# Optimization experiments

Measured on AMD Instinct MI355X. Metric: run time of the kernel, lower is better.

The kernel has to match this reference:

```python
import jax, jax.numpy as jnp
import numpy as np

HEADS = 2
K_HOP = 2
RATIO = 0.8
NEG_SLOPE = 0.01


def seg_softmax(logits, seg, num_seg):
    # torch_geometric.utils.softmax: numerically stable segment softmax
    m = jax.ops.segment_max(logits, seg, num_segments=num_seg)
    e = jnp.exp(logits - m[seg])
    d = jax.ops.segment_sum(e, seg, num_segments=num_seg)
    return e / d[seg]


def _attention(key_value, query, seg, num_seg, Wk, W1, W2, W3):
    # Attention.forward with enable_BN=False; weights stored [in,out] so x@W == torch Linear
    a = key_value @ Wk
    h = jnp.concatenate([a, query, a - query, a * query], axis=-1)  # [N,4H]
    h = jax.nn.leaky_relu(h @ W1, NEG_SLOPE)
    h = jax.nn.leaky_relu(h @ W2, NEG_SLOPE)
    h = jax.nn.leaky_relu(h @ W3, NEG_SLOPE)  # [N,1]
    return seg_softmax(h[:, 0], seg, num_seg)[:, None]  # att_weights [N,1]


def setup_inputs():
    key = jax.random.key(0)
    ks = jax.random.split(key, 10)
    B, n, H, epg = 64, 64, 128, 2048
    N = B * n
    x = jax.random.normal(ks[0], (N, H), jnp.float32)
    src = jax.random.randint(ks[1], (B, epg), 0, n)
    dst = jax.random.randint(ks[2], (B, epg), 0, n)
    off = (jnp.arange(B) * n)[:, None]
    edge_index = jnp.stack([(src + off).reshape(-1), (dst + off).reshape(-1)], 0)
    edge_weight = jax.random.uniform(ks[3], (B * epg,), jnp.float32)
    target_x = jax.random.normal(ks[4], (B, H), jnp.float32)
    batch_ixs = jnp.repeat(jnp.arange(B), n)
    s = lambda i, sh: jax.random.normal(ks[i], sh, jnp.float32) / np.sqrt(sh[-2])
    # index 0=cluster_att, 1=query_att, 2=cluster_att2, 3=query_att2
    att_Wk = s(5, (4, H, H))
    att_W1 = s(6, (4, 4 * H, 2 * H))
    att_W2 = s(7, (4, 2 * H, H))
    att_W3 = s(8, (4, H, 1))
    lin_W = s(9, (HEADS, H, H))
    return dict(x=x, edge_index=edge_index, edge_weight=edge_weight, target_x=target_x,
                batch_ixs=batch_ixs, att_Wk=att_Wk, att_W1=att_W1, att_W2=att_W2,
                att_W3=att_W3, lin_W=lin_W)


def reference(x, edge_index, edge_weight, target_x, batch_ixs, att_Wk, att_W1, att_W2, att_W3, lin_W):
    N, H = x.shape
    B = target_x.shape[0]
    n = N // B
    # ---- gcn_norm with self loops (fill 1.0) ----
    loop = jnp.arange(N)
    row = jnp.concatenate([edge_index[0], loop])
    col = jnp.concatenate([edge_index[1], loop])
    w = jnp.concatenate([edge_weight, jnp.ones((N,), edge_weight.dtype)])
    deg = jax.ops.segment_sum(w, col, num_segments=N)
    dinv = jnp.where(deg > 0, jax.lax.rsqrt(jnp.maximum(deg, 1e-12)), 0.0)
    ew = dinv[row] * w * dinv[col]  # [L]
    # ---- k-hop propagation ----
    def hop(v):
        return jax.ops.segment_sum(v[row] * ew[:, None], col, num_segments=N)
    x_q = x
    for _ in range(K_HOP):
        x_q = hop(x_q)
    qt = target_x[batch_ixs]  # repeat_interleave by per-graph counts (sorted batch)
    # ---- multi-head edge attention (reuse_att_w=True, dropout=0 -> E identical per head) ----
    f1 = _attention(x, x_q, batch_ixs, B, att_Wk[0], att_W1[0], att_W2[0], att_W3[0])
    f2 = _attention(x, qt, batch_ixs, B, att_Wk[1], att_W1[1], att_W2[1], att_W3[1])
    E = jax.nn.leaky_relu(f1[col] + f2[row], NEG_SLOPE)  # [L,1]
    E = seg_softmax(E[:, 0], col, N)[:, None]
    x_c = jnp.zeros_like(x)
    E_g = jnp.zeros((row.shape[0], 1), x.dtype)
    agg = jax.ops.segment_sum(x[row] * E, col, num_segments=N)
    for h in range(HEADS):
        x_c = x_c + jax.nn.leaky_relu(x + agg @ lin_W[h], NEG_SLOPE)
        E_g = E_g + E
    x_c = x_c / HEADS
    E_g = E_g / HEADS
    # ---- second k-hop + cluster scoring ----
    x_q2 = x_c
    for _ in range(K_HOP):
        x_q2 = hop(x_q2)
    g1 = _attention(x_c, x_q2, batch_ixs, B, att_Wk[2], att_W1[2], att_W2[2], att_W3[2])
    g2 = _attention(x_c, qt, batch_ixs, B, att_Wk[3], att_W1[3], att_W2[3], att_W3[3])
    # stack over heads then mean == g1+g2 (same attention modules reused per head)
    cluster_score = seg_softmax((g1 + g2)[:, 0], batch_ixs, B)  # [N]
    # ---- per-graph topk (ratio) ----
    kk = int(np.ceil(RATIO * n))
    _, idx = jax.lax.top_k(cluster_score.reshape(B, n), kk)  # descending, matches PyG topk
    perm = (idx + (jnp.arange(B) * n)[:, None]).reshape(-1)  # [Nk]
    x_out = x[perm] * cluster_score[perm][:, None]
    batch_out = batch_ixs[perm]
    # ---- S^T A S (dense equivalent of SparseTensor triple product) ----
    A_d = jnp.zeros((N, N), x.dtype).at[row, col].add(ew)
    S_d = jnp.zeros((N, N), x.dtype).at[row, col].add(E_g[:, 0])
    S_p = S_d[:, perm]  # S[:, perm] -> [N, Nk]
    A2 = S_p.T @ (A_d @ S_p)  # [Nk, Nk]
    Nk = perm.shape[0]
    A2 = A2.at[jnp.arange(Nk), jnp.arange(Nk)].set(1.0)  # fill_diag(1.0)
    return x_out, A2, batch_out, perm
```

## Files before the change

kernel.cpp:

```cpp
#include <hip/hip_runtime.h>

#define KK 52
#define NKOUT 3328
#define NEG 0.01f

typedef __attribute__((ext_vector_type(8))) __bf16 bf16x8;
typedef __attribute__((ext_vector_type(16))) float floatx16;

__device__ __forceinline__ float lrelu(float v){ return v > 0.f ? v : NEG*v; }

#define SW(r, ko) ((r)*40 + ((ko) ^ ((((r)>>3)&3) << 3)))

__device__ __forceinline__ void split_store8(const float* vv, __bf16* P0, __bf16* P1, __bf16* P2, int addr){
  bf16x8 p1, p2, p3;
  #pragma unroll
  for (int j = 0; j < 8; j++){
    __bf16 b1 = (__bf16)vv[j];
    float r1 = vv[j] - (float)b1;
    __bf16 b2 = (__bf16)r1;
    float r2 = r1 - (float)b2;
    p1[j] = b1; p2[j] = b2; p3[j] = (__bf16)r2;
  }
  *(bf16x8*)(P0 + addr) = p1;
  *(bf16x8*)(P1 + addr) = p2;
  *(bf16x8*)(P2 + addr) = p3;
}

__device__ __forceinline__ void mfma6(const __bf16* A0, const __bf16* A1, const __bf16* A2,
                                      const __bf16* B0, const __bf16* B1, const __bf16* B2,
                                      int aoff, int boff, floatx16* acc){
  bf16x8 a1 = *(const bf16x8*)(A0 + aoff);
  bf16x8 a2 = *(const bf16x8*)(A1 + aoff);
  bf16x8 a3 = *(const bf16x8*)(A2 + aoff);
  bf16x8 b1 = *(const bf16x8*)(B0 + boff);
  bf16x8 b2 = *(const bf16x8*)(B1 + boff);
  bf16x8 b3 = *(const bf16x8*)(B2 + boff);
  floatx16 c = *acc;
  c = __builtin_amdgcn_mfma_f32_32x32x16_bf16(a1,b1,c,0,0,0);
  c = __builtin_amdgcn_mfma_f32_32x32x16_bf16(a1,b2,c,0,0,0);
  c = __builtin_amdgcn_mfma_f32_32x32x16_bf16(a2,b1,c,0,0,0);
  c = __builtin_amdgcn_mfma_f32_32x32x16_bf16(a1,b3,c,0,0,0);
  c = __builtin_amdgcn_mfma_f32_32x32x16_bf16(a3,b1,c,0,0,0);
  c = __builtin_amdgcn_mfma_f32_32x32x16_bf16(a2,b2,c,0,0,0);
  *acc = c;
}

__device__ __forceinline__ void g_gemm(const float* A0, int ldA,
                                       const float* __restrict__ W0, int ldW, int K,
                                       __bf16* pb, floatx16* oA, floatx16* oB){
  __bf16 *As0 = pb, *As1 = pb+2560, *As2 = pb+5120;
  __bf16 *Bs0 = pb+7680, *Bs1 = pb+12800, *Bs2 = pb+17920;
  int tid = threadIdx.x;
  int sar = tid >> 2, sako = (tid & 3)*8;
  int bn = tid & 127, bk = (tid >> 7)*16;
  int wv_ = tid >> 6, L = tid & 63, m = L & 31, half = L >> 5;
  int rA = 32*(wv_ & 1) + m, rB0 = (wv_ >> 1)*32 + m, rB1 = rB0 + 64;
  const float* arow = A0 + (size_t)sar*ldA;
  floatx16 accA, accB;
  #pragma unroll
  for (int i = 0; i < 16; i++){ accA[i] = 0.f; accB[i] = 0.f; }
  float ra[8], wv[16];
  {
    float4 v0 = *(const float4*)(arow + sako);
    float4 v1 = *(const float4*)(arow + sako + 4);
    ra[0]=v0.x; ra[1]=v0.y; ra[2]=v0.z; ra[3]=v0.w; ra[4]=v1.x; ra[5]=v1.y; ra[6]=v1.z; ra[7]=v1.w;
    #pragma unroll
    for (int j = 0; j < 16; j++) wv[j] = W0[(size_t)(bk + j)*ldW + bn];
  }
  for (int k0 = 0; k0 < K; k0 += 32){
    split_store8(ra, As0, As1, As2, SW(sar, sako));
    split_store8(wv,     Bs0, Bs1, Bs2, SW(bn, bk));
    split_store8(wv + 8, Bs0, Bs1, Bs2, SW(bn, bk + 8));
    __syncthreads();
    int k1 = k0 + 32;
    float ra2[8], wv2[16];
    if (k1 < K){
      float4 v0 = *(const float4*)(arow + k1 + sako);
      float4 v1 = *(const float4*)(arow + k1 + sako + 4);
      ra2[0]=v0.x; ra2[1]=v0.y; ra2[2]=v0.z; ra2[3]=v0.w; ra2[4]=v1.x; ra2[5]=v1.y; ra2[6]=v1.z; ra2[7]=v1.w;
      #pragma unroll
      for (int j = 0; j < 16; j++) wv2[j] = W0[(size_t)(k1 + bk + j)*ldW + bn];
    }
    #pragma unroll
    for (int kg = 0; kg < 2; kg++){
      int ko = kg*16 + half*8;
      mfma6(As0,As1,As2, Bs0,Bs1,Bs2, SW(rA,ko), SW(rB0,ko), &accA);
      mfma6(As0,As1,As2, Bs0,Bs1,Bs2, SW(rA,ko), SW(rB1,ko), &accB);
    }
    __syncthreads();
    if (k1 < K){
      #pragma unroll
      for (int j = 0; j < 8; j++) ra[j] = ra2[j];
      #pragma unroll
      for (int j = 0; j < 16; j++) wv[j] = wv2[j];
    }
  }
  *oA = accA; *oB = accB;
}

__device__ __forceinline__ void g_gemm64(const float* __restrict__ A0, int ldA,
                                         const float* __restrict__ W0, int ldW, int K,
                                         __bf16* pb, floatx16* oC){
  __bf16 *As0 = pb, *As1 = pb+2560, *As2 = pb+5120;
  __bf16 *Bs0 = pb+7680, *Bs1 = pb+10240, *Bs2 = pb+12800;
  int tid = threadIdx.x;
  int sar = tid >> 2, sako = (tid & 3)*8;
  int bn = tid & 63, bk = (tid >> 6)*8;
  int wv_ = tid >> 6, L = tid & 63, m = L & 31, half = L >> 5;
  int rA = 32*(wv_ & 1) + m, rB = 32*(wv_ >> 1) + m;
  const float* arow = A0 + (size_t)sar*ldA;
  floatx16 acc;
  #pragma unroll
  for (int i = 0; i < 16; i++) acc[i] = 0.f;
  float ra[8], wv[8];
  {
    float4 v0 = *(const float4*)(arow + sako);
    float4 v1 = *(const float4*)(arow + sako + 4);
    ra[0]=v0.x; ra[1]=v0.y; ra[2]=v0.z; ra[3]=v0.w; ra[4]=v1.x; ra[5]=v1.y; ra[6]=v1.z; ra[7]=v1.w;
    #pragma unroll
    for (int j = 0; j < 8; j++) wv[j] = W0[(size_t)(bk + j)*ldW + bn];
  }
  for (int k0 = 0; k0 < K; k0 += 32){
    split_store8(ra, As0, As1, As2, SW(sar, sako));
    split_store8(wv, Bs0, Bs1, Bs2, SW(bn, bk));
    __syncthreads();
    int k1 = k0 + 32;
    float ra2[8], wv2[8];
    if (k1 < K){
      float4 v0 = *(const float4*)(arow + k1 + sako);
      float4 v1 = *(const float4*)(arow + k1 + sako + 4);
      ra2[0]=v0.x; ra2[1]=v0.y; ra2[2]=v0.z; ra2[3]=v0.w; ra2[4]=v1.x; ra2[5]=v1.y; ra2[6]=v1.z; ra2[7]=v1.w;
      #pragma unroll
      for (int j = 0; j < 8; j++) wv2[j] = W0[(size_t)(k1 + bk + j)*ldW + bn];
    }
    #pragma unroll
    for (int kg = 0; kg < 2; kg++){
      int ko = kg*16 + half*8;
      mfma6(As0,As1,As2, Bs0,Bs1,Bs2, SW(rA,ko), SW(rB,ko), &acc);
    }
    __syncthreads();
    if (k1 < K){
      #pragma unroll
      for (int j = 0; j < 8; j++){ ra[j] = ra2[j]; wv[j] = wv2[j]; }
    }
  }
  *oC = acc;
}

__device__ __forceinline__ void g_gemm_h64(const float* __restrict__ arow, const float* __restrict__ qrow,
                                           const float* __restrict__ W1fz, int colbase,
                                           __bf16* pb, floatx16* oC){
  __bf16 *As0 = pb, *As1 = pb+2560, *As2 = pb+5120;
  __bf16 *Bs0 = pb+7680, *Bs1 = pb+10240, *Bs2 = pb+12800;
  int tid = threadIdx.x;
  int sar = tid >> 2, sako = (tid & 3)*8;
  int bn = tid & 63, bk = (tid >> 6)*8;
  int col = colbase + bn;
  int wv_ = tid >> 6, L = tid & 63, m = L & 31, half = L >> 5;
  int rA = 32*(wv_ & 1) + m, rB = 32*(wv_ >> 1) + m;
  auto loadA = [&](int k0, float* r){
    int seg = k0 >> 7, kl = (k0 & 127) + sako;
    if (seg == 0){
      float4 a0 = *(const float4*)(arow + kl), a1 = *(const float4*)(arow + kl + 4);
      r[0]=a0.x; r[1]=a0.y; r[2]=a0.z; r[3]=a0.w; r[4]=a1.x; r[5]=a1.y; r[6]=a1.z; r[7]=a1.w;
    } else if (seg == 1){
      float4 q0 = *(const float4*)(qrow + kl), q1 = *(const float4*)(qrow + kl + 4);
      r[0]=q0.x; r[1]=q0.y; r[2]=q0.z; r[3]=q0.w; r[4]=q1.x; r[5]=q1.y; r[6]=q1.z; r[7]=q1.w;
    } else {
      float4 a0 = *(const float4*)(arow + kl), a1 = *(const float4*)(arow + kl + 4);
      float4 q0 = *(const float4*)(qrow + kl), q1 = *(const float4*)(qrow + kl + 4);
      r[0]=a0.x*q0.x; r[1]=a0.y*q0.y; r[2]=a0.z*q0.z; r[3]=a0.w*q0.w;
      r[4]=a1.x*q1.x; r[5]=a1.y*q1.y; r[6]=a1.z*q1.z; r[7]=a1.w*q1.w;
    }
  };
  auto loadB = [&](int k0, float* r){
    #pragma unroll
    for (int j = 0; j < 8; j++) r[j] = W1fz[(size_t)(k0 + bk + j)*256 + col];
  };
  floatx16 acc;
  #pragma unroll
  for (int i = 0; i < 16; i++) acc[i] = 0.f;
  float ra[8], wv[8];
  loadA(0, ra); loadB(0, wv);
  for (int k0 = 0; k0 < 384; k0 += 32){
    split_store8(ra, As0, As1, As2, SW(sar, sako));
    split_store8(wv, Bs0, Bs1, Bs2, SW(bn, bk));
    __syncthreads();
    int k1 = k0 + 32;
    float ra2[8], wv2[8];
    if (k1 < 384){ loadA(k1, ra2); loadB(k1, wv2); }
    #pragma unroll
    for (int kg = 0; kg < 2; kg++){
      int ko = kg*16 + half*8;
      mfma6(As0,As1,As2, Bs0,Bs1,Bs2, SW(rA,ko), SW(rB,ko), &acc);
    }
    __syncthreads();
    if (k1 < 384){
      #pragma unroll
      for (int j = 0; j < 8; j++){ ra[j] = ra2[j]; wv[j] = wv2[j]; }
    }
  }
  *oC = acc;
}

__device__ __forceinline__ void c_write(floatx16 accA, floatx16 accB, float* C0, int ldC, int act){
  int tid = threadIdx.x, wv_ = tid >> 6, L = tid & 63, m = L & 31, half = L >> 5;
  int rB0 = (wv_ >> 1)*32 + m, rB1 = rB0 + 64;
  int row0 = 32*(wv_ & 1) + 4*half;
  #pragma unroll
  for (int reg = 0; reg < 16; reg++){
    int row = row0 + (reg & 3) + 8*(reg >> 2);
    float va = accA[reg], vb = accB[reg];
    if (act){ va = lrelu(va); vb = lrelu(vb); }
    C0[(size_t)row*ldC + rB0] = va;
    C0[(size_t)row*ldC + rB1] = vb;
  }
}

__device__ __forceinline__ void c_write64(floatx16 acc, float* C0, int ldC, int act){
  int tid = threadIdx.x, wv_ = tid >> 6, L = tid & 63, m = L & 31, half = L >> 5;
  int col = 32*(wv_ >> 1) + m;
  int row0 = 32*(wv_ & 1) + 4*half;
  #pragma unroll
  for (int reg = 0; reg < 16; reg++){
    int row = row0 + (reg & 3) + 8*(reg >> 2);
    float v = acc[reg];
    if (act) v = lrelu(v);
    C0[(size_t)row*ldC + col] = v;
  }
}

__device__ __forceinline__ void hop2_run(const float* A, const float* VfullL, int ldV,
                                         const float* srcG, float* dstG, int dstOff,
                                         float* Vt, float* Tt, int fbeg, int fend){
  int tid = threadIdx.x;
  int tc = (tid & 31)*2, tf = (tid >> 5)*4;
  for (int f0 = fbeg; f0 < fend; f0 += 32){
    if (!VfullL){
      for (int o = tid; o < 2048; o += 256){
        int r = o >> 5, f = o & 31;
        Vt[o] = srcG[r*128 + f0 + f];
      }
      __syncthreads();
    }
    float a00,a01,a02,a03,a10,a11,a12,a13;
    a00=a01=a02=a03=a10=a11=a12=a13=0.f;
    for (int r = 0; r < 64; r++){
      float x0 = A[r*64 + tc], x1 = A[r*64 + tc + 1];
      float4 v4 = VfullL ? *(const float4*)&VfullL[r*ldV + f0 + tf]
                         : *(const float4*)&Vt[r*32 + tf];
      a00 += x0*v4.x; a01 += x0*v4.y; a02 += x0*v4.z; a03 += x0*v4.w;
      a10 += x1*v4.x; a11 += x1*v4.y; a12 += x1*v4.z; a13 += x1*v4.w;
    }
    *(float4*)&Tt[tc*32 + tf]     = make_float4(a00,a01,a02,a03);
    *(float4*)&Tt[(tc+1)*32 + tf] = make_float4(a10,a11,a12,a13);
    __syncthreads();
    a00=a01=a02=a03=a10=a11=a12=a13=0.f;
    for (int r = 0; r < 64; r++){
      float x0 = A[r*64 + tc], x1 = A[r*64 + tc + 1];
      float4 v4 = *(const float4*)&Tt[r*32 + tf];
      a00 += x0*v4.x; a01 += x0*v4.y; a02 += x0*v4.z; a03 += x0*v4.w;
      a10 += x1*v4.x; a11 += x1*v4.y; a12 += x1*v4.z; a13 += x1*v4.w;
    }
    *(float4*)(dstG + tc*128 + dstOff + f0 + tf)     = make_float4(a00,a01,a02,a03);
    *(float4*)(dstG + (tc+1)*128 + dstOff + f0 + tf) = make_float4(a10,a11,a12,a13);
    __syncthreads();
  }
}

__global__ __launch_bounds__(256) void k_p0(const int* __restrict__ ei, const float* __restrict__ ew,
                                            const float* __restrict__ x, const float* __restrict__ Wk,
                                            const float* __restrict__ W1, const float* __restrict__ linW,
                                            float* A_g, float* M_g, float* xq, float* a_buf, float* W1f,
                                            float* xl0, float* xl1, float* outA2){
  __shared__ __align__(16) char POOL[57856];
  float* pf = (float*)POOL;
  __bf16* pb = (__bf16*)POOL;
  int blk = blockIdx.x, tid = threadIdx.x;
  if (blk < 128){
    int b = blk >> 1, fh = blk & 1;
    float* Ws = pf; float* Mc = pf + 4096; float* dv = pf + 8192;
    for (int i = tid; i < 4096; i += 256){ Ws[i] = 0.f; Mc[i] = 0.f; }
    __syncthreads();
    const int* r0 = ei + b*2048;
    const int* c0 = ei + 64*2048 + b*2048;
    const float* w0 = ew + b*2048;
    int base = b*64;
    for (int e = tid; e < 2048; e += 256){
      int r = r0[e] - base, c = c0[e] - base;
      atomicAdd(&Ws[r*64 + c], w0[e]);
      atomicAdd(&Mc[r*64 + c], 1.f);
    }
    if (tid < 64){ atomicAdd(&Ws[tid*65], 1.f); atomicAdd(&Mc[tid*65], 1.f); }
    __syncthreads();
    if (tid < 64){
      float d = 0.f;
      for (int r = 0; r < 64; r++) d += Ws[r*64 + tid];
      dv[tid] = d > 0.f ? rsqrtf(fmaxf(d, 1e-12f)) : 0.f;
    }
    __syncthreads();
    for (int i = tid; i < 4096; i += 256){
      int r = i >> 6, c = i & 63;
      float a = dv[r]*Ws[i]*dv[c];
      Ws[i] = a;
      if (fh == 0){
        A_g[b*4096 + i] = a;
        M_g[b*4096 + i] = Mc[i];
      }
    }
    __syncthreads();
    hop2_run(Ws, nullptr, 0, x + (size_t)b*8192, xq + (size_t)b*8192, 0, pf + 8256, pf + 10304,
             fh*64, fh*64 + 64);
  } else if (blk < 256){
    int idx = blk - 128, z = idx >> 6, b = idx & 63;
    floatx16 cA, cB;
    g_gemm(x + (size_t)b*8192, 128, Wk + (size_t)z*16384, 128, 128, pb, &cA, &cB);
    c_write(cA, cB, a_buf + (size_t)z*524288 + (size_t)b*8192, 128, 0);
  } else if (blk < 320){
    int idx0 = (blk - 256)*6144;
    for (int i = tid; i < 6144; i += 256){
      int g = idx0 + i;
      int zz = g / 98304;
      int r = g - zz*98304;
      int kr = r >> 8, c = r & 255;
      const float* Wz = W1 + (size_t)zz*131072;
      float v;
      if (kr < 128)       v = Wz[kr*256 + c] + Wz[(kr + 256)*256 + c];
      else if (kr < 256)  v = Wz[kr*256 + c] - Wz[(kr + 128)*256 + c];
      else                v = Wz[(kr + 128)*256 + c];
      W1f[g] = v;
    }
  } else if (blk < 3024){
    float4* p = (float4*)outA2;
    int base = (blk - 320)*1024 + tid;
    #pragma unroll
    for (int i = 0; i < 4; i++) p[base + i*256] = make_float4(0.f,0.f,0.f,0.f);
  } else {
    int idx = blk - 3024, z = idx >> 6, b = idx & 63;
    floatx16 cA, cB;
    g_gemm(x + (size_t)b*8192, 128, linW + (size_t)z*16384, 128, 128, pb, &cA, &cB);
    c_write(cA, cB, (z ? xl1 : xl0) + (size_t)b*8192, 128, 0);
  }
}

__global__ __launch_bounds__(256) void k_h1(const float* __restrict__ a_buf, const float* __restrict__ q0,
                                            const float* __restrict__ tgt, const float* __restrict__ W1fp,
                                            float* h1){
  __shared__ __align__(16) char POOL[30720];
  __bf16* pb = (__bf16*)POOL;
  int blk = blockIdx.x, tid = threadIdx.x;
  int b = blk >> 3, z = (blk >> 2) & 1, nq = blk & 3;
  int sar = tid >> 2;
  const float* arow = a_buf + (size_t)z*524288 + ((size_t)b*64 + sar)*128;
  const float* qrow = z ? (tgt + (size_t)b*128) : (q0 + ((size_t)b*64 + sar)*128);
  floatx16 c;
  g_gemm_h64(arow, qrow, W1fp + (size_t)z*98304, nq*64, pb, &c);
  c_write64(c, h1 + (size_t)z*1048576 + (size_t)b*16384 + nq*64, 256, 1);
}

__global__ __launch_bounds__(256) void k_w2p(const float* __restrict__ h1, const float* __restrict__ W2,
                                             const float* __restrict__ W3, float* __restrict__ lp){
  __shared__ __align__(16) char POOL[30720];
  __shared__ float lgp[128];
  __bf16* pb = (__bf16*)POOL;
  int blk = blockIdx.x, tid = threadIdx.x;
  int b = blk >> 2, z = (blk >> 1) & 1, nh = blk & 1;
  floatx16 c;
  g_gemm64(h1 + (size_t)z*1048576 + (size_t)b*16384, 256,
           W2 + (size_t)z*32768 + nh*64, 128, 256, pb, &c);
  int wv_ = tid >> 6, L = tid & 63, m = L & 31, half = L >> 5;
  int col = 32*(wv_ >> 1) + m;
  float w = W3[z*128 + nh*64 + col];
  float v[16];
  #pragma unroll
  for (int reg = 0; reg < 16; reg++) v[reg] = lrelu(c[reg])*w;
  #pragma unroll
  for (int off = 1; off < 32; off <<= 1)
    #pragma unroll
    for (int reg = 0; reg < 16; reg++) v[reg] += __shfl_xor(v[reg], off);
  if (m == 0){
    #pragma unroll
    for (int reg = 0; reg < 16; reg++) lgp[wv_*32 + half*16 + reg] = v[reg];
  }
  __syncthreads();
  if (tid < 64){
    int row = tid, rh = row >> 5, rem = row & 31;
    int hf = (rem >> 2) & 1, rg = (rem & 3) + 4*(rem >> 3);
    float p = lgp[rh*32 + hf*16 + rg] + lgp[(rh + 2)*32 + hf*16 + rg];
    lp[(z*2 + nh)*4096 + b*64 + row] = p;
  }
}

__global__ __launch_bounds__(256) void k_edgehop(const float* __restrict__ M_g, const float* __restrict__ lp,
                                                 const float* __restrict__ x, const float* __restrict__ xl0g,
                                                 const float* __restrict__ xl1g, const float* __restrict__ A_g,
                                                 float* S_g, float* xcb, float* xq2){
  __shared__ __align__(16) float Mc[4096];
  __shared__ __align__(16) float xh[4096];
  __shared__ __align__(16) float xl0h[4096];
  __shared__ __align__(16) float xl1h[4096];
  __shared__ __align__(16) float Ab[4096];
  __shared__ __align__(16) float Tt[2048];
  __shared__ float f1s[64], f2s[64];
  int blk = blockIdx.x, b = blk >> 1, fh = blk & 1, tid = threadIdx.x;
  int foff = fh*64;
  for (int i = tid; i < 4096; i += 256) Mc[i] = M_g[b*4096 + i];
  for (int o = tid*4; o < 4096; o += 1024){
    int r = o >> 6, f = o & 63;
    *(float4*)&xh[o]   = *(const float4*)(x    + (size_t)b*8192 + r*128 + foff + f);
    *(float4*)&xl0h[o] = *(const float4*)(xl0g + (size_t)b*8192 + r*128 + foff + f);
    *(float4*)&xl1h[o] = *(const float4*)(xl1g + (size_t)b*8192 + r*128 + foff + f);
  }
  if (tid < 128){
    int z = tid >> 6, r = tid & 63;
    float d = lp[(z*2)*4096 + b*64 + r] + lp[(z*2 + 1)*4096 + b*64 + r];
    float l = lrelu(d);
    float mx = l;
    #pragma unroll
    for (int off = 32; off; off >>= 1) mx = fmaxf(mx, __shfl_xor(mx, off));
    float e = expf(l - mx);
    float s = e;
    #pragma unroll
    for (int off = 32; off; off >>= 1) s += __shfl_xor(s, off);
    (z ? f2s : f1s)[r] = e/s;
  }
  __syncthreads();
  {
    int c = tid >> 2, sub = tid & 3;
    float m = -1e30f;
    for (int r = sub; r < 64; r += 4)
      if (Mc[r*64 + c] > 0.f) m = fmaxf(m, lrelu(f1s[c] + f2s[r]));
    m = fmaxf(m, __shfl_xor(m, 1));
    m = fmaxf(m, __shfl_xor(m, 2));
    float s = 0.f;
    for (int r = sub; r < 64; r += 4){
      float mc = Mc[r*64 + c];
      if (mc > 0.f) s += mc*expf(lrelu(f1s[c] + f2s[r]) - m);
    }
    s += __shfl_xor(s, 1);
    s += __shfl_xor(s, 2);
    for (int r = sub; r < 64; r += 4){
      float mc = Mc[r*64 + c];
      float v = 0.f;
      if (mc > 0.f) v = mc*expf(lrelu(f1s[c] + f2s[r]) - m)/s;
      Mc[r*64 + c] = v;
    }
  }
  __syncthreads();
  if (fh == 0)
    for (int i = tid; i < 4096; i += 256) S_g[b*4096 + i] = Mc[i];
  {
    int tc = (tid & 15)*4, tf = (tid >> 4)*4;
    float a0[4][4], a1[4][4];
    #pragma unroll
    for (int i = 0; i < 4; i++)
      #pragma unroll
      for (int j = 0; j < 4; j++){ a0[i][j] = 0.f; a1[i][j] = 0.f; }
    for (int r = 0; r < 64; r++){
      float4 e4 = *(const float4*)&Mc[r*64 + tc];
      float4 p0 = *(const float4*)&xl0h[r*64 + tf];
      float4 p1 = *(const float4*)&xl1h[r*64 + tf];
      float e_[4] = {e4.x,e4.y,e4.z,e4.w};
      float p0_[4] = {p0.x,p0.y,p0.z,p0.w};
      float p1_[4] = {p1.x,p1.y,p1.z,p1.w};
      #pragma unroll
      for (int ci = 0; ci < 4; ci++)
        #pragma unroll
        for (int fj = 0; fj < 4; fj++){
          a0[ci][fj] += e_[ci]*p0_[fj];
          a1[ci][fj] += e_[ci]*p1_[fj];
        }
    }
    __syncthreads();
    #pragma unroll
    for (int ci = 0; ci < 4; ci++){
      int c = tc + ci;
      float4 xv = *(const float4*)&xh[c*64 + tf];
      float4 o;
      o.x = 0.5f*(lrelu(xv.x + a0[ci][0]) + lrelu(xv.x + a1[ci][0]));
      o.y = 0.5f*(lrelu(xv.y + a0[ci][1]) + lrelu(xv.y + a1[ci][1]));
      o.z = 0.5f*(lrelu(xv.z + a0[ci][2]) + lrelu(xv.z + a1[ci][2]));
      o.w = 0.5f*(lrelu(xv.w + a0[ci][3]) + lrelu(xv.w + a1[ci][3]));
      *(float4*)&xh[c*64 + tf] = o;
      *(float4*)(xcb + (size_t)b*8192 + c*128 + foff + tf) = o;
    }
  }
  for (int i = tid*4; i < 4096; i += 1024)
    *(float4*)&Ab[i] = *(const float4*)(A_g + b*4096 + i);
  __syncthreads();
  hop2_run(Ab, xh, 64, nullptr, xq2 + (size_t)b*8192, foff, Tt, Tt, 0, 64);
}

__global__ __launch_bounds__(256) void k_wkg(const float* __restrict__ xcb, const float* __restrict__ Wkg,
                                             float* a_buf){
  __shared__ __align__(16) char POOL[30720];
  __bf16* pb = (__bf16*)POOL;
  int blk = blockIdx.x;
  int b = blk >> 2, z = (blk >> 1) & 1, nh = blk & 1;
  floatx16 c;
  g_gemm64(xcb + (size_t)b*8192, 128, Wkg + (size_t)z*16384 + nh*64, 128, 128, pb, &c);
  c_write64(c, a_buf + (size_t)z*524288 + (size_t)b*8192 + nh*64, 128, 0);
}

__global__ __launch_bounds__(256) void k_A2c(const float* __restrict__ lp, const float* __restrict__ x,
                                             const float* __restrict__ A_g, const float* __restrict__ S_g,
                                             float* outA2, float* outX, float* outB, float* outP){
  __shared__ __align__(16) float At[64*68];
  __shared__ __align__(16) float Sp[64*56];
  __shared__ __align__(16) float Tq[64*56];
  __shared__ int pi[64];
  __shared__ float pv[64];
  int b = blockIdx.x, tid = threadIdx.x;
  if (tid < 64){
    int lane = tid;
    float f[2];
    #pragma unroll
    for (int z = 0; z < 2; z++){
      float d = lp[(z*2)*4096 + b*64 + lane] + lp[(z*2 + 1)*4096 + b*64 + lane];
      float l = lrelu(d);
      float mx = l;
      #pragma unroll
      for (int off = 32; off; off >>= 1) mx = fmaxf(mx, __shfl_xor(mx, off));
      float e = expf(l - mx);
      float sm = e;
      #pragma unroll
      for (int off = 32; off; off >>= 1) sm += __shfl_xor(sm, off);
      f[z] = e/sm;
    }
    float l = f[0] + f[1];
    float m = l;
    #pragma unroll
    for (int off = 32; off; off >>= 1) m = fmaxf(m, __shfl_xor(m, off));
    float e = expf(l - m);
    float sm = e;
    #pragma unroll
    for (int off = 32; off; off >>= 1) sm += __shfl_xor(sm, off);
    float v = e/sm;
    int idx = lane;
    #pragma unroll
    for (int k = 2; k <= 64; k <<= 1){
      #pragma unroll
      for (int j = k >> 1; j > 0; j >>= 1){
        float ov = __shfl_xor(v, j);
        int   oi = __shfl_xor(idx, j);
        bool ascBlock = (lane & k) == 0;
        bool iAmLow   = (lane & j) == 0;
        bool otherPrec = (ov > v) || (ov == v && oi < idx);
        bool take = (ascBlock == iAmLow) ? otherPrec : !otherPrec;
        if (take){ v = ov; idx = oi; }
      }
    }
    pi[lane] = idx; pv[lane] = v;
    if (lane < KK){
      outB[b*KK + lane] = (float)b;
      outP[b*KK + lane] = (float)(b*64 + idx);
    }
  }
  __syncthreads();
  for (int o = tid*4; o < KK*128; o += 1024){
    int j = o >> 7, f = o & 127;
    float4 xv = *(const float4*)(x + ((size_t)b*64 + pi[j])*128 + f);
    float sv = pv[j];
    *(float4*)(outX + (size_t)b*KK*128 + o) = make_float4(xv.x*sv, xv.y*sv, xv.z*sv, xv.w*sv);
  }
  for (int idx = tid; idx < 4096; idx += 256){
    int i = idx >> 6, k = idx & 63;
    At[k*68 + i] = A_g[b*4096 + idx];
  }
  for (int idx = tid; idx < 4096; idx += 256){
    int k = idx >> 6, t = idx & 63;
    if (t < 56) Sp[k*56 + t] = (t < KK) ? S_g[b*4096 + k*64 + pi[t]] : 0.f;
  }
  __syncthreads();
  if (tid < 224){
    int i0 = (tid/14)*4, t0 = (tid % 14)*4;
    float acc[4][4];
    #pragma unroll
    for (int a = 0; a < 4; a++)
      #pragma unroll
      for (int c = 0; c < 4; c++) acc[a][c] = 0.f;
    for (int k = 0; k < 64; k++){
      float4 a4 = *(const float4*)&At[k*68 + i0];
      float4 s4 = *(const float4*)&Sp[k*56 + t0];
      float a_[4] = {a4.x,a4.y,a4.z,a4.w};
      float s_[4] = {s4.x,s4.y,s4.z,s4.w};
      #pragma unroll
      for (int ii = 0; ii < 4; ii++)
        #pragma unroll
        for (int tt = 0; tt < 4; tt++) acc[ii][tt] += a_[ii]*s_[tt];
    }
    #pragma unroll
    for (int ii = 0; ii < 4; ii++)
      *(float4*)&Tq[(i0+ii)*56 + t0] = make_float4(acc[ii][0],acc[ii][1],acc[ii][2],acc[ii][3]);
  }
  __syncthreads();
  if (tid < 169){
    int a0 = (tid/13)*4, t0 = (tid % 13)*4;
    float acc[4][4];
    #pragma unroll
    for (int a = 0; a < 4; a++)
      #pragma unroll
      for (int c = 0; c < 4; c++) acc[a][c] = 0.f;
    for (int i = 0; i < 64; i++){
      float4 s4 = *(const float4*)&Sp[i*56 + a0];
      float4 t4 = *(const float4*)&Tq[i*56 + t0];
      float s_[4] = {s4.x,s4.y,s4.z,s4.w};
      float t_[4] = {t4.x,t4.y,t4.z,t4.w};
      #pragma unroll
      for (int aa = 0; aa < 4; aa++)
        #pragma unroll
        for (int tt = 0; tt < 4; tt++) acc[aa][tt] += s_[aa]*t_[tt];
    }
    #pragma unroll
    for (int aa = 0; aa < 4; aa++){
      int a = a0 + aa;
      float4 o;
      o.x = (a == t0    ) ? 1.f : acc[aa][0];
      o.y = (a == t0 + 1) ? 1.f : acc[aa][1];
      o.z = (a == t0 + 2) ? 1.f : acc[aa][2];
      o.w = (a == t0 + 3) ? 1.f : acc[aa][3];
      *(float4*)(outA2 + (size_t)(b*KK + a)*NKOUT + b*KK + t0) = o;
    }
  }
}

extern "C" void kernel_launch(void* const* d_in, const int* in_sizes, int n_in,
                              void* d_out, int out_size, void* d_ws, size_t ws_size,
                              hipStream_t stream){
  const float* x    = (const float*)d_in[0];
  const int*   ei   = (const int*)d_in[1];
  const float* ew   = (const float*)d_in[2];
  const float* tgt  = (const float*)d_in[3];
  const float* Wk   = (const float*)d_in[5];
  const float* W1   = (const float*)d_in[6];
  const float* W2   = (const float*)d_in[7];
  const float* W3   = (const float*)d_in[8];
  const float* linW = (const float*)d_in[9];
  float* out = (float*)d_out;

  float* wf   = (float*)d_ws;
  float* A_g  = wf;
  float* M_g  = wf + 262144;
  float* S_g  = wf + 524288;
  float* xq   = wf + 786432;
  float* xq2  = wf + 1310720;
  float* xl0  = wf + 1835008;
  float* xcb  = wf + 2359296;
  float* a_buf= wf + 2883584;
  float* h1   = wf + 3932160;
  float* lp   = wf + 6029312;
  float* W1f  = wf + 6045696;
  float* xl1  = wf + 6438912;

  float* outX  = out;
  float* outA2 = out + 425984;
  float* outB  = out + 425984 + 11075584;
  float* outP  = outB + NKOUT;

  k_p0<<<dim3(3152), dim3(256), 0, stream>>>(ei, ew, x, Wk, W1, linW, A_g, M_g, xq, a_buf, W1f,
                                             xl0, xl1, outA2);
  k_h1<<<dim3(512), dim3(256), 0, stream>>>(a_buf, xq, tgt, W1f, h1);
  k_w2p<<<dim3(256), dim3(256), 0, stream>>>(h1, W2, W3, lp);
  k_edgehop<<<dim3(128), dim3(256), 0, stream>>>(M_g, lp, x, xl0, xl1, A_g, S_g, xcb, xq2);
  k_wkg<<<dim3(256), dim3(256), 0, stream>>>(xcb, Wk + 2*16384, a_buf);
  k_h1<<<dim3(512), dim3(256), 0, stream>>>(a_buf, xq2, tgt, W1f + 2*98304, h1);
  k_w2p<<<dim3(256), dim3(256), 0, stream>>>(h1, W2 + 2*32768, W3 + 2*128, lp);
  k_A2c<<<dim3(64), dim3(256), 0, stream>>>(lp, x, A_g, S_g, outA2, outX, outB, outP);
}
```

Measured before the change: 211.9 us.

## Pre-split weights and h1 into transposed bf16 planes to skip per-tile splitting

Weight matrices W1 (folded), W2 and the cluster Wk are converted once in the prologue kernel into three transposed bf16 residual planes. The GEMMs then load them as contiguous 16-byte vectors instead of strided scalar fp32 loads followed by a per-tile split. The first MLP layer now writes its activated output h1 directly as bf16 planes, so the second layer loads both operands pre-split. This removes repeated split arithmetic and uncoalesced weight reads, at the cost of extra prologue blocks and tripled plane storage.

```diff
diff --git a/kernel.cpp b/kernel.cpp
--- a/kernel.cpp
+++ b/kernel.cpp
@@ -98,9 +98,9 @@
   *oA = accA; *oB = accB;
 }
 
-__device__ __forceinline__ void g_gemm64(const float* __restrict__ A0, int ldA,
-                                         const float* __restrict__ W0, int ldW, int K,
-                                         __bf16* pb, floatx16* oC){
+__device__ __forceinline__ void g_gemm64_bp(const float* __restrict__ A0, int ldA,
+                                            const __bf16* __restrict__ Bp, int bps, int ldKb, int K,
+                                            __bf16* pb, floatx16* oC){
   __bf16 *As0 = pb, *As1 = pb+2560, *As2 = pb+5120;
   __bf16 *Bs0 = pb+7680, *Bs1 = pb+10240, *Bs2 = pb+12800;
   int tid = threadIdx.x;
@@ -109,29 +109,34 @@
   int wv_ = tid >> 6, L = tid & 63, m = L & 31, half = L >> 5;
   int rA = 32*(wv_ & 1) + m, rB = 32*(wv_ >> 1) + m;
   const float* arow = A0 + (size_t)sar*ldA;
+  const __bf16* brow = Bp + (size_t)bn*ldKb + bk;
   floatx16 acc;
   #pragma unroll
   for (int i = 0; i < 16; i++) acc[i] = 0.f;
-  float ra[8], wv[8];
+  float ra[8]; bf16x8 rb[3];
   {
     float4 v0 = *(const float4*)(arow + sako);
     float4 v1 = *(const float4*)(arow + sako + 4);
     ra[0]=v0.x; ra[1]=v0.y; ra[2]=v0.z; ra[3]=v0.w; ra[4]=v1.x; ra[5]=v1.y; ra[6]=v1.z; ra[7]=v1.w;
-    #pragma unroll
-    for (int j = 0; j < 8; j++) wv[j] = W0[(size_t)(bk + j)*ldW + bn];
+    rb[0] = *(const bf16x8*)(brow);
+    rb[1] = *(const bf16x8*)(brow + bps);
+    rb[2] = *(const bf16x8*)(brow + 2*bps);
   }
   for (int k0 = 0; k0 < K; k0 += 32){
     split_store8(ra, As0, As1, As2, SW(sar, sako));
-    split_store8(wv, Bs0, Bs1, Bs2, SW(bn, bk));
+    *(bf16x8*)(Bs0 + SW(bn, bk)) = rb[0];
+    *(bf16x8*)(Bs1 + SW(bn, bk)) = rb[1];
+    *(bf16x8*)(Bs2 + SW(bn, bk)) = rb[2];
     __syncthreads();
     int k1 = k0 + 32;
-    float ra2[8], wv2[8];
+    float ra2[8]; bf16x8 rb2[3];
     if (k1 < K){
       float4 v0 = *(const float4*)(arow + k1 + sako);
       float4 v1 = *(const float4*)(arow + k1 + sako + 4);
       ra2[0]=v0.x; ra2[1]=v0.y; ra2[2]=v0.z; ra2[3]=v0.w; ra2[4]=v1.x; ra2[5]=v1.y; ra2[6]=v1.z; ra2[7]=v1.w;
-      #pragma unroll
-      for (int j = 0; j < 8; j++) wv2[j] = W0[(size_t)(k1 + bk + j)*ldW + bn];
+      rb2[0] = *(const bf16x8*)(brow + k1);
+      rb2[1] = *(const bf16x8*)(brow + bps + k1);
+      rb2[2] = *(const bf16x8*)(brow + 2*bps + k1);
     }
     #pragma unroll
     for (int kg = 0; kg < 2; kg++){
@@ -141,23 +146,80 @@
     __syncthreads();
     if (k1 < K){
       #pragma unroll
-      for (int j = 0; j < 8; j++){ ra[j] = ra2[j]; wv[j] = wv2[j]; }
+      for (int j = 0; j < 8; j++) ra[j] = ra2[j];
+      rb[0]=rb2[0]; rb[1]=rb2[1]; rb[2]=rb2[2];
     }
   }
   *oC = acc;
 }
 
+__device__ __forceinline__ void g_gemm64_abp(const __bf16* __restrict__ Ap, int aps, int ldKa,
+                                             const __bf16* __restrict__ Bp, int bps, int ldKb, int K,
+                                             __bf16* pb, floatx16* oC){
+  __bf16 *As0 = pb, *As1 = pb+2560, *As2 = pb+5120;
+  __bf16 *Bs0 = pb+7680, *Bs1 = pb+10240, *Bs2 = pb+12800;
+  int tid = threadIdx.x;
+  int sar = tid >> 2, sako = (tid & 3)*8;
+  int bn = tid & 63, bk = (tid >> 6)*8;
+  int wv_ = tid >> 6, L = tid & 63, m = L & 31, half = L >> 5;
+  int rA = 32*(wv_ & 1) + m, rB = 32*(wv_ >> 1) + m;
+  const __bf16* arow = Ap + (size_t)sar*ldKa + sako;
+  const __bf16* brow = Bp + (size_t)bn*ldKb + bk;
+  floatx16 acc;
+  #pragma unroll
+  for (int i = 0; i < 16; i++) acc[i] = 0.f;
+  bf16x8 ra[3], rb[3];
+  {
+    ra[0] = *(const bf16x8*)(arow);
+    ra[1] = *(const bf16x8*)(arow + aps);
+    ra[2] = *(const bf16x8*)(arow + 2*aps);
+    rb[0] = *(const bf16x8*)(brow);
+    rb[1] = *(const bf16x8*)(brow + bps);
+    rb[2] = *(const bf16x8*)(brow + 2*bps);
+  }
+  for (int k0 = 0; k0 < K; k0 += 32){
+    *(bf16x8*)(As0 + SW(sar, sako)) = ra[0];
+    *(bf16x8*)(As1 + SW(sar, sako)) = ra[1];
+    *(bf16x8*)(As2 + SW(sar, sako)) = ra[2];
+    *(bf16x8*)(Bs0 + SW(bn, bk)) = rb[0];
+    *(bf16x8*)(Bs1 + SW(bn, bk)) = rb[1];
+    *(bf16x8*)(Bs2 + SW(bn, bk)) = rb[2];
+    __syncthreads();
+    int k1 = k0 + 32;
+    bf16x8 ra2[3], rb2[3];
+    if (k1 < K){
+      ra2[0] = *(const bf16x8*)(arow + k1);
+      ra2[1] = *(const bf16x8*)(arow + aps + k1);
+      ra2[2] = *(const bf16x8*)(arow + 2*aps + k1);
+      rb2[0] = *(const bf16x8*)(brow + k1);
+      rb2[1] = *(const bf16x8*)(brow + bps + k1);
+      rb2[2] = *(const bf16x8*)(brow + 2*bps + k1);
+    }
+    #pragma unroll
+    for (int kg = 0; kg < 2; kg++){
+      int ko = kg*16 + half*8;
+      mfma6(As0,As1,As2, Bs0,Bs1,Bs2, SW(rA,ko), SW(rB,ko), &acc);
+    }
+    __syncthreads();
+    if (k1 < K){
+      ra[0]=ra2[0]; ra[1]=ra2[1]; ra[2]=ra2[2];
+      rb[0]=rb2[0]; rb[1]=rb2[1]; rb[2]=rb2[2];
+    }
+  }
+  *oC = acc;
+}
+
 __device__ __forceinline__ void g_gemm_h64(const float* __restrict__ arow, const float* __restrict__ qrow,
-                                           const float* __restrict__ W1fz, int colbase,
+                                           const __bf16* __restrict__ Bp,
                                            __bf16* pb, floatx16* oC){
   __bf16 *As0 = pb, *As1 = pb+2560, *As2 = pb+5120;
   __bf16 *Bs0 = pb+7680, *Bs1 = pb+10240, *Bs2 = pb+12800;
   int tid = threadIdx.x;
   int sar = tid >> 2, sako = (tid & 3)*8;
   int bn = tid & 63, bk = (tid >> 6)*8;
-  int col = colbase + bn;
   int wv_ = tid >> 6, L = tid & 63, m = L & 31, half = L >> 5;
   int rA = 32*(wv_ & 1) + m, rB = 32*(wv_ >> 1) + m;
+  const __bf16* brow = Bp + (size_t)bn*384 + bk;
   auto loadA = [&](int k0, float* r){
     int seg = k0 >> 7, kl = (k0 & 127) + sako;
     if (seg == 0){
@@ -173,22 +235,28 @@
       r[4]=a1.x*q1.x; r[5]=a1.y*q1.y; r[6]=a1.z*q1.z; r[7]=a1.w*q1.w;
     }
   };
-  auto loadB = [&](int k0, float* r){
-    #pragma unroll
-    for (int j = 0; j < 8; j++) r[j] = W1fz[(size_t)(k0 + bk + j)*256 + col];
-  };
   floatx16 acc;
   #pragma unroll
   for (int i = 0; i < 16; i++) acc[i] = 0.f;
-  float ra[8], wv[8];
-  loadA(0, ra); loadB(0, wv);
+  float ra[8]; bf16x8 rb[3];
+  loadA(0, ra);
+  rb[0] = *(const bf16x8*)(brow);
+  rb[1] = *(const bf16x8*)(brow + 98304);
+  rb[2] = *(const bf16x8*)(brow + 196608);
   for (int k0 = 0; k0 < 384; k0 += 32){
     split_store8(ra, As0, As1, As2, SW(sar, sako));
-    split_store8(wv, Bs0, Bs1, Bs2, SW(bn, bk));
+    *(bf16x8*)(Bs0 + SW(bn, bk)) = rb[0];
+    *(bf16x8*)(Bs1 + SW(bn, bk)) = rb[1];
+    *(bf16x8*)(Bs2 + SW(bn, bk)) = rb[2];
     __syncthreads();
     int k1 = k0 + 32;
-    float ra2[8], wv2[8];
-    if (k1 < 384){ loadA(k1, ra2); loadB(k1, wv2); }
+    float ra2[8]; bf16x8 rb2[3];
+    if (k1 < 384){
+      loadA(k1, ra2);
+      rb2[0] = *(const bf16x8*)(brow + k1);
+      rb2[1] = *(const bf16x8*)(brow + 98304 + k1);
+      rb2[2] = *(const bf16x8*)(brow + 196608 + k1);
+    }
     #pragma unroll
     for (int kg = 0; kg < 2; kg++){
       int ko = kg*16 + half*8;
@@ -197,7 +265,8 @@
     __syncthreads();
     if (k1 < 384){
       #pragma unroll
-      for (int j = 0; j < 8; j++){ ra[j] = ra2[j]; wv[j] = wv2[j]; }
+      for (int j = 0; j < 8; j++) ra[j] = ra2[j];
+      rb[0]=rb2[0]; rb[1]=rb2[1]; rb[2]=rb2[2];
     }
   }
   *oC = acc;
@@ -227,6 +296,23 @@
     float v = acc[reg];
     if (act) v = lrelu(v);
     C0[(size_t)row*ldC + col] = v;
+  }
+}
+
+__device__ __forceinline__ void c_write64_planes(floatx16 acc, __bf16* P){
+  int tid = threadIdx.x, wv_ = tid >> 6, L = tid & 63, m = L & 31, half = L >> 5;
+  int col = 32*(wv_ >> 1) + m;
+  int row0 = 32*(wv_ & 1) + 4*half;
+  #pragma unroll
+  for (int reg = 0; reg < 16; reg++){
+    int row = row0 + (reg & 3) + 8*(reg >> 2);
+    float v = lrelu(acc[reg]);
+    __bf16 b1 = (__bf16)v;
+    float r1 = v - (float)b1;
+    __bf16 b2 = (__bf16)r1;
+    __bf16 b3 = (__bf16)(r1 - (float)b2);
+    int o = row*256 + col;
+    P[o] = b1; P[16384 + o] = b2; P[32768 + o] = b3;
   }
 }
 
@@ -268,10 +354,20 @@
   }
 }
 
+__device__ __forceinline__ void split_t_lds(float v, __bf16* Ls, int idx){
+  __bf16 b1 = (__bf16)v;
+  float r1 = v - (float)b1;
+  __bf16 b2 = (__bf16)r1;
+  __bf16 b3 = (__bf16)(r1 - (float)b2);
+  Ls[idx] = b1; Ls[4224 + idx] = b2; Ls[8448 + idx] = b3;
+}
+
 __global__ __launch_bounds__(256) void k_p0(const int* __restrict__ ei, const float* __restrict__ ew,
                                             const float* __restrict__ x, const float* __restrict__ Wk,
-                                            const float* __restrict__ W1, const float* __restrict__ linW,
-                                            float* A_g, float* M_g, float* xq, float* a_buf, float* W1f,
+                                            const float* __restrict__ W1, const float* __restrict__ W2,
+                                            const float* __restrict__ linW,
+                                            float* A_g, float* M_g, float* xq, float* a_buf,
+                                            __bf16* W1fp, __bf16* W2p, __bf16* Wkgp,
                                             float* xl0, float* xl1, float* outA2){
   __shared__ __align__(16) char POOL[57856];
   float* pf = (float*)POOL;
@@ -316,27 +412,71 @@
     floatx16 cA, cB;
     g_gemm(x + (size_t)b*8192, 128, Wk + (size_t)z*16384, 128, 128, pb, &cA, &cB);
     c_write(cA, cB, a_buf + (size_t)z*524288 + (size_t)b*8192, 128, 0);
-  } else if (blk < 320){
-    int idx0 = (blk - 256)*6144;
-    for (int i = tid; i < 6144; i += 256){
-      int g = idx0 + i;
-      int zz = g / 98304;
-      int r = g - zz*98304;
-      int kr = r >> 8, c = r & 255;
-      const float* Wz = W1 + (size_t)zz*131072;
+  } else if (blk < 352){
+    __bf16* Ls = (__bf16*)POOL;
+    int t = blk - 256, z = t/24, tt = t%24, k0 = (tt >> 2)*64, c0 = (tt & 3)*64;
+    const float* Wz = W1 + (size_t)z*131072;
+    for (int i = tid; i < 4096; i += 256){
+      int kk = i >> 6, cc = i & 63, kr = k0 + kk, c = c0 + cc;
       float v;
       if (kr < 128)       v = Wz[kr*256 + c] + Wz[(kr + 256)*256 + c];
       else if (kr < 256)  v = Wz[kr*256 + c] - Wz[(kr + 128)*256 + c];
       else                v = Wz[(kr + 128)*256 + c];
-      W1f[g] = v;
-    }
-  } else if (blk < 3024){
+      split_t_lds(v, Ls, cc*66 + kk);
+    }
+    __syncthreads();
+    __bf16* outp = W1fp + (size_t)z*294912;
+    for (int i = tid; i < 4096; i += 256){
+      int cc = i >> 6, kk = i & 63;
+      int o = (c0 + cc)*384 + k0 + kk;
+      int li = cc*66 + kk;
+      outp[o] = Ls[li];
+      outp[98304 + o] = Ls[4224 + li];
+      outp[196608 + o] = Ls[8448 + li];
+    }
+  } else if (blk < 384){
+    __bf16* Ls = (__bf16*)POOL;
+    int t = blk - 352, z = t >> 3, tt = t & 7, k0 = (tt >> 1)*64, c0 = (tt & 1)*64;
+    const float* Wz = W2 + (size_t)z*32768;
+    for (int i = tid; i < 4096; i += 256){
+      int kk = i >> 6, cc = i & 63;
+      split_t_lds(Wz[(k0 + kk)*128 + c0 + cc], Ls, cc*66 + kk);
+    }
+    __syncthreads();
+    __bf16* outp = W2p + (size_t)z*98304;
+    for (int i = tid; i < 4096; i += 256){
+      int cc = i >> 6, kk = i & 63;
+      int o = (c0 + cc)*256 + k0 + kk;
+      int li = cc*66 + kk;
+      outp[o] = Ls[li];
+      outp[32768 + o] = Ls[4224 + li];
+      outp[65536 + o] = Ls[8448 + li];
+    }
+  } else if (blk < 392){
+    __bf16* Ls = (__bf16*)POOL;
+    int t = blk - 384, z = t >> 2, tt = t & 3, k0 = (tt >> 1)*64, c0 = (tt & 1)*64;
+    const float* Wz = Wk + (size_t)(2 + z)*16384;
+    for (int i = tid; i < 4096; i += 256){
+      int kk = i >> 6, cc = i & 63;
+      split_t_lds(Wz[(k0 + kk)*128 + c0 + cc], Ls, cc*66 + kk);
+    }
+    __syncthreads();
+    __bf16* outp = Wkgp + (size_t)z*49152;
+    for (int i = tid; i < 4096; i += 256){
+      int cc = i >> 6, kk = i & 63;
+      int o = (c0 + cc)*128 + k0 + kk;
+      int li = cc*66 + kk;
+      outp[o] = Ls[li];
+      outp[16384 + o] = Ls[4224 + li];
+      outp[32768 + o] = Ls[8448 + li];
+    }
+  } else if (blk < 3096){
     float4* p = (float4*)outA2;
-    int base = (blk - 320)*1024 + tid;
+    int base = (blk - 392)*1024 + tid;
     #pragma unroll
     for (int i = 0; i < 4; i++) p[base + i*256] = make_float4(0.f,0.f,0.f,0.f);
   } else {
-    int idx = blk - 3024, z = idx >> 6, b = idx & 63;
+    int idx = blk - 3096, z = idx >> 6, b = idx & 63;
     floatx16 cA, cB;
     g_gemm(x + (size_t)b*8192, 128, linW + (size_t)z*16384, 128, 128, pb, &cA, &cB);
     c_write(cA, cB, (z ? xl1 : xl0) + (size_t)b*8192, 128, 0);
@@ -344,8 +484,8 @@
 }
 
 __global__ __launch_bounds__(256) void k_h1(const float* __restrict__ a_buf, const float* __restrict__ q0,
-                                            const float* __restrict__ tgt, const float* __restrict__ W1fp,
-                                            float* h1){
+                                            const float* __restrict__ tgt, const __bf16* __restrict__ W1fp,
+                                            __bf16* h1p){
   __shared__ __align__(16) char POOL[30720];
   __bf16* pb = (__bf16*)POOL;
   int blk = blockIdx.x, tid = threadIdx.x;
@@ -354,11 +494,11 @@
   const float* arow = a_buf + (size_t)z*524288 + ((size_t)b*64 + sar)*128;
   const float* qrow = z ? (tgt + (size_t)b*128) : (q0 + ((size_t)b*64 + sar)*128);
   floatx16 c;
-  g_gemm_h64(arow, qrow, W1fp + (size_t)z*98304, nq*64, pb, &c);
-  c_write64(c, h1 + (size_t)z*1048576 + (size_t)b*16384 + nq*64, 256, 1);
-}
-
-__global__ __launch_bounds__(256) void k_w2p(const float* __restrict__ h1, const float* __restrict__ W2,
+  g_gemm_h64(arow, qrow, W1fp + (size_t)z*294912 + (size_t)nq*64*384, pb, &c);
+  c_write64_planes(c, h1p + (size_t)(z*64 + b)*3*16384 + nq*64);
+}
+
+__global__ __launch_bounds__(256) void k_w2p(const __bf16* __restrict__ h1p, const __bf16* __restrict__ W2p,
                                              const float* __restrict__ W3, float* __restrict__ lp){
   __shared__ __align__(16) char POOL[30720];
   __shared__ float lgp[128];
@@ -366,8 +506,8 @@
   int blk = blockIdx.x, tid = threadIdx.x;
   int b = blk >> 2, z = (blk >> 1) & 1, nh = blk & 1;
   floatx16 c;
-  g_gemm64(h1 + (size_t)z*1048576 + (size_t)b*16384, 256,
-           W2 + (size_t)z*32768 + nh*64, 128, 256, pb, &c);
+  g_gemm64_abp(h1p + (size_t)(z*64 + b)*3*16384, 16384, 256,
+               W2p + (size_t)z*98304 + (size_t)nh*64*256, 32768, 256, 256, pb, &c);
   int wv_ = tid >> 6, L = tid & 63, m = L & 31, half = L >> 5;
   int col = 32*(wv_ >> 1) + m;
   float w = W3[z*128 + nh*64 + col];
@@ -491,14 +631,15 @@
   hop2_run(Ab, xh, 64, nullptr, xq2 + (size_t)b*8192, foff, Tt, Tt, 0, 64);
 }
 
-__global__ __launch_bounds__(256) void k_wkg(const float* __restrict__ xcb, const float* __restrict__ Wkg,
+__global__ __launch_bounds__(256) void k_wkg(const float* __restrict__ xcb, const __bf16* __restrict__ Wkgp,
                                              float* a_buf){
   __shared__ __align__(16) char POOL[30720];
   __bf16* pb = (__bf16*)POOL;
   int blk = blockIdx.x;
   int b = blk >> 2, z = (blk >> 1) & 1, nh = blk & 1;
   floatx16 c;
-  g_gemm64(xcb + (size_t)b*8192, 128, Wkg + (size_t)z*16384 + nh*64, 128, 128, pb, &c);
+  g_gemm64_bp(xcb + (size_t)b*8192, 128,
+              Wkgp + (size_t)z*49152 + (size_t)nh*64*128, 16384, 128, 128, pb, &c);
   c_write64(c, a_buf + (size_t)z*524288 + (size_t)b*8192 + nh*64, 128, 0);
 }
 
@@ -647,23 +788,25 @@
   float* xl0  = wf + 1835008;
   float* xcb  = wf + 2359296;
   float* a_buf= wf + 2883584;
-  float* h1   = wf + 3932160;
-  float* lp   = wf + 6029312;
-  float* W1f  = wf + 6045696;
-  float* xl1  = wf + 6438912;
+  float* lp   = wf + 3932160;
+  float* xl1  = wf + 3948544;
+  __bf16* W1fp = (__bf16*)(wf + 4472832);
+  __bf16* W2p  = (__bf16*)(wf + 5062656);
+  __bf16* Wkgp = (__bf16*)(wf + 5259264);
+  __bf16* h1p  = (__bf16*)(wf + 5308416);
 
   float* outX  = out;
   float* outA2 = out + 425984;
   float* outB  = out + 425984 + 11075584;
   float* outP  = outB + NKOUT;
 
-  k_p0<<<dim3(3152), dim3(256), 0, stream>>>(ei, ew, x, Wk, W1, linW, A_g, M_g, xq, a_buf, W1f,
-                                             xl0, xl1, outA2);
-  k_h1<<<dim3(512), dim3(256), 0, stream>>>(a_buf, xq, tgt, W1f, h1);
-  k_w2p<<<dim3(256), dim3(256), 0, stream>>>(h1, W2, W3, lp);
+  k_p0<<<dim3(3224), dim3(256), 0, stream>>>(ei, ew, x, Wk, W1, W2, linW, A_g, M_g, xq, a_buf,
+                                             W1fp, W2p, Wkgp, xl0, xl1, outA2);
+  k_h1<<<dim3(512), dim3(256), 0, stream>>>(a_buf, xq, tgt, W1fp, h1p);
+  k_w2p<<<dim3(256), dim3(256), 0, stream>>>(h1p, W2p, W3, lp);
   k_edgehop<<<dim3(128), dim3(256), 0, stream>>>(M_g, lp, x, xl0, xl1, A_g, S_g, xcb, xq2);
-  k_wkg<<<dim3(256), dim3(256), 0, stream>>>(xcb, Wk + 2*16384, a_buf);
-  k_h1<<<dim3(512), dim3(256), 0, stream>>>(a_buf, xq2, tgt, W1f + 2*98304, h1);
-  k_w2p<<<dim3(256), dim3(256), 0, stream>>>(h1, W2 + 2*32768, W3 + 2*128, lp);
+  k_wkg<<<dim3(256), dim3(256), 0, stream>>>(xcb, Wkgp, a_buf);
+  k_h1<<<dim3(512), dim3(256), 0, stream>>>(a_buf, xq2, tgt, W1fp + 2*294912, h1p);
+  k_w2p<<<dim3(256), dim3(256), 0, stream>>>(h1p, W2p + 2*98304, W3 + 2*128, lp);
   k_A2c<<<dim3(64), dim3(256), 0, stream>>>(lp, x, A_g, S_g, outA2, outX, outB, outP);
 }
```

After: 220.4 us. 1.04x slower.
